# Optimization experiments

Hardware: AMD Instinct MI355X
Metric: run time of the kernel (lower is better)

## Reference

```python
import jax, jax.numpy as jnp
import numpy as np

N_NODES = 50000


def _sage_conv(x, src, dst, Wl, bl, Wr):
    # mean aggregation of neighbor (source) features at destination nodes
    msg = x[src]                                              # [E, d]
    agg = jax.ops.segment_sum(msg, dst, num_segments=N_NODES)  # [N, d]
    cnt = jax.ops.segment_sum(jnp.ones((src.shape[0],), x.dtype), dst,
                              num_segments=N_NODES)            # [N]
    agg = agg / jnp.clip(cnt, 1.0)[:, None]
    # lin_l(aggregated) + lin_r(self), bias only on lin_l (PyG default)
    return agg @ Wl + bl + x @ Wr


def setup_inputs() -> dict:
    key = jax.random.key(0)
    ks = jax.random.split(key, 8)
    d = 128
    E = 800000
    x = jax.random.normal(ks[0], (N_NODES, d), dtype=jnp.float32)
    edge_index = jax.random.randint(ks[1], (2, E), 0, N_NODES, dtype=jnp.int64)
    s1 = 1.0 / np.sqrt(d)
    s2 = 1.0 / np.sqrt(32)
    return {
        "x": x,
        "edge_index": edge_index,
        "W1l": jax.random.normal(ks[2], (d, 32), jnp.float32) * s1,
        "b1": jnp.zeros((32,), jnp.float32),
        "W1r": jax.random.normal(ks[3], (d, 32), jnp.float32) * s1,
        "W2l": jax.random.normal(ks[4], (32, 32), jnp.float32) * s2,
        "b2": jnp.zeros((32,), jnp.float32),
        "W2r": jax.random.normal(ks[5], (32, 32), jnp.float32) * s2,
    }


def reference(x, edge_index, W1l, b1, W1r, W2l, b2, W2r):
    src, dst = edge_index[0], edge_index[1]
    h = jax.nn.relu(_sage_conv(x, src, dst, W1l, b1, W1r))
    return _sage_conv(h, src, dst, W2l, b2, W2r)
```

## Files before the change

### kernel.cpp

```cpp
#include <hip/hip_runtime.h>


#define N_NODES 50000
#define NB 782
#define BKS 64
#define GB 256
#define CAPE 1280

__global__ __launch_bounds__(256) void kproj(
    const float* __restrict__ in, const float* __restrict__ Wl,
    const float* __restrict__ Wr, float* __restrict__ z, int N, int K) {
  __shared__ float xs[64 * 68];
  __shared__ float ws[64 * 64];
  const int t = threadIdx.x;
  const int n0 = blockIdx.x * 64;
  const int nvalid = (N - n0) < 64 ? (N - n0) : 64;

  const int tx = t & 15, ty = t >> 4;
  const int c0 = tx * 4;
  const int nl = ty * 4;

  float acc[4][4];
#pragma unroll
  for (int i = 0; i < 4; i++)
#pragma unroll
    for (int j = 0; j < 4; j++) acc[i][j] = 0.f;

  for (int kc = 0; kc < K; kc += 64) {
    const int KC = (K - kc) < 64 ? (K - kc) : 64;
    for (int i = t; i < KC * 32; i += 256) {
      int k = i >> 5, c = i & 31;
      ws[k * 64 + c] = Wl[(size_t)(kc + k) * 32 + c];
      ws[k * 64 + 32 + c] = Wr[(size_t)(kc + k) * 32 + c];
    }
    {
      const int kq = KC >> 2;
      const int sh = (KC == 64) ? 4 : 3;
      const int lim = nvalid * kq;
      for (int i = t; i < lim; i += 256) {
        int n = i >> sh, q = i & (kq - 1);
        float4 v = *(const float4*)(in + (size_t)(n0 + n) * K + kc + q * 4);
        *(float4*)(xs + n * 68 + q * 4) = v;
      }
    }
    __syncthreads();

    const float* x0 = xs + (nl + 0) * 68;
    const float* x1 = xs + (nl + 1) * 68;
    const float* x2 = xs + (nl + 2) * 68;
    const float* x3 = xs + (nl + 3) * 68;
    for (int k = 0; k < KC; k += 4) {
      float4 xa = *(const float4*)(x0 + k);
      float4 xb = *(const float4*)(x1 + k);
      float4 xc = *(const float4*)(x2 + k);
      float4 xd = *(const float4*)(x3 + k);
#pragma unroll
      for (int kk = 0; kk < 4; kk++) {
        float4 w = *(const float4*)(ws + (k + kk) * 64 + c0);
        float va = ((const float*)&xa)[kk];
        float vb = ((const float*)&xb)[kk];
        float vc = ((const float*)&xc)[kk];
        float vd = ((const float*)&xd)[kk];
        acc[0][0] += va * w.x; acc[0][1] += va * w.y;
        acc[0][2] += va * w.z; acc[0][3] += va * w.w;
        acc[1][0] += vb * w.x; acc[1][1] += vb * w.y;
        acc[1][2] += vb * w.z; acc[1][3] += vb * w.w;
        acc[2][0] += vc * w.x; acc[2][1] += vc * w.y;
        acc[2][2] += vc * w.z; acc[2][3] += vc * w.w;
        acc[3][0] += vd * w.x; acc[3][1] += vd * w.y;
        acc[3][2] += vd * w.z; acc[3][3] += vd * w.w;
      }
    }
    __syncthreads();
  }
#pragma unroll
  for (int i = 0; i < 4; i++) {
    int node = n0 + nl + i;
    if (node < N) {
      float4 v = make_float4(acc[i][0], acc[i][1], acc[i][2], acc[i][3]);
      *(float4*)(z + (size_t)node * 64 + c0) = v;
    }
  }
}

__global__ __launch_bounds__(256) void k_bcount(const int* __restrict__ dst,
                                                int* __restrict__ blkhist,
                                                int E, int chunk) {
  __shared__ int h[NB];
  const int t = threadIdx.x, b = blockIdx.x;
  for (int i = t; i < NB; i += 256) h[i] = 0;
  __syncthreads();
  const int e0 = b * chunk;
  int e1 = e0 + chunk;
  if (e1 > E) e1 = E;
  for (int e = e0 + t; e < e1; e += 256) atomicAdd(&h[dst[e] >> 6], 1);
  __syncthreads();
  for (int i = t; i < NB; i += 256) blkhist[b * NB + i] = h[i];
}

__global__ __launch_bounds__(256) void k_bscan_col(int* __restrict__ blkhist,
                                                   int* __restrict__ tot) {
  const int c = blockIdx.x * 256 + threadIdx.x;
  if (c >= NB) return;
  int run = 0;
  for (int b = 0; b < GB; b += 8) {
    int v[8];
#pragma unroll
    for (int i = 0; i < 8; i++) v[i] = blkhist[(size_t)(b + i) * NB + c];
#pragma unroll
    for (int i = 0; i < 8; i++) {
      blkhist[(size_t)(b + i) * NB + c] = run;
      run += v[i];
    }
  }
  tot[c] = run;
}

__global__ __launch_bounds__(256) void k_bscan_bb(const int* __restrict__ tot,
                                                  int* __restrict__ bb, int E) {
  __shared__ int t4[1024];
  __shared__ int sc[256];
  const int t = threadIdx.x;
  for (int c = t; c < 1024; c += 256) t4[c] = (c < NB) ? tot[c] : 0;
  __syncthreads();
  const int base = 4 * t;
  int v0 = t4[base], v1 = t4[base + 1], v2 = t4[base + 2], v3 = t4[base + 3];
  int s = v0 + v1 + v2 + v3;
  sc[t] = s;
  __syncthreads();
  for (int off = 1; off < 256; off <<= 1) {
    int tmp = (t >= off) ? sc[t - off] : 0;
    __syncthreads();
    sc[t] += tmp;
    __syncthreads();
  }
  const int excl = sc[t] - s;
  if (base < NB) bb[base] = excl;
  if (base + 1 < NB) bb[base + 1] = excl + v0;
  if (base + 2 < NB) bb[base + 2] = excl + v0 + v1;
  if (base + 3 < NB) bb[base + 3] = excl + v0 + v1 + v2;
  if (t == 0) bb[NB] = E;
}

__global__ __launch_bounds__(256) void k_bscatter(
    const int* __restrict__ src, const int* __restrict__ dst,
    const int* __restrict__ blkhist, const int* __restrict__ bb,
    int* __restrict__ ebuf, int E, int chunk) {
  __shared__ int cur[NB];
  const int t = threadIdx.x, b = blockIdx.x;
  for (int i = t; i < NB; i += 256) cur[i] = bb[i] + blkhist[(size_t)b * NB + i];
  __syncthreads();
  const int e0 = b * chunk;
  int e1 = e0 + chunk;
  if (e1 > E) e1 = E;
  for (int e = e0 + t; e < e1; e += 256) {
    int d = dst[e], s = src[e];
    int pos = atomicAdd(&cur[d >> 6], 1);
    ebuf[pos] = (s << 6) | (d & 63);
  }
}

__global__ __launch_bounds__(512) void k_fagg1(
    const float* __restrict__ zc, const int* __restrict__ ebuf,
    const int* __restrict__ bb, const float* __restrict__ b1,
    const float* __restrict__ W2l, const float* __restrict__ W2r,
    float* __restrict__ z2, int N) {
  __shared__ int lds_e[CAPE];
  __shared__ int lds_s[CAPE];
  __shared__ int deg[BKS];
  __shared__ int cur[BKS];
  __shared__ int off[BKS];
  __shared__ float w2p[32 * 64];
  __shared__ float bsh[32];
  const int t = threadIdx.x;
  const int k = blockIdx.x;
  const int r0 = bb[k], r1 = bb[k + 1];
  int ne = r1 - r0;
  if (ne > CAPE) ne = CAPE;

  for (int i = t; i < ne; i += 512) lds_e[i] = ebuf[r0 + i];
  if (t < BKS) deg[t] = 0;
  for (int i = t; i < 2048; i += 512) {
    int jj = i >> 6, c = i & 63;
    w2p[i] = (c < 32) ? W2l[jj * 32 + c] : W2r[jj * 32 + (c - 32)];
  }
  if (t < 32) bsh[t] = b1[t];
  __syncthreads();

  for (int i = t; i < ne; i += 512) atomicAdd(&deg[lds_e[i] & 63], 1);
  __syncthreads();

  if (t < 64) {
    int d = deg[t];
    int x = d;
#pragma unroll
    for (int o = 1; o < 64; o <<= 1) {
      int y = __shfl_up(x, o, 64);
      if (t >= o) x += y;
    }
    off[t] = x - d;
    cur[t] = x - d;
  }
  __syncthreads();

  for (int i = t; i < ne; i += 512) {
    int v = lds_e[i];
    int p = atomicAdd(&cur[v & 63], 1);
    lds_s[p] = v >> 6;
  }
  __syncthreads();

  const int g = t >> 5, j = t & 31;
  const int n0 = k << 6;
#pragma unroll
  for (int i = 0; i < 4; i++) {
    const int nl = g * 4 + i;
    const int node = n0 + nl;
    if (node >= N) break;
    const int a = off[nl];
    const int dg = deg[nl];
    const int b = a + dg;
    float a0 = 0.f, a1 = 0.f, a2 = 0.f, a3 = 0.f;
    int e = a;
    for (; e + 4 <= b; e += 4) {
      int s0 = lds_s[e], s1 = lds_s[e + 1], s2 = lds_s[e + 2], s3 = lds_s[e + 3];
      a0 += zc[(size_t)s0 * 64 + j];
      a1 += zc[(size_t)s1 * 64 + j];
      a2 += zc[(size_t)s2 * 64 + j];
      a3 += zc[(size_t)s3 * 64 + j];
    }
    for (; e < b; ++e) a0 += zc[(size_t)lds_s[e] * 64 + j];
    float sum = (a0 + a1) + (a2 + a3);
    float h = sum / (float)(dg > 1 ? dg : 1) + bsh[j] +
              zc[(size_t)node * 64 + 32 + j];
    h = fmaxf(h, 0.f);
    float p0 = 0.f, p1 = 0.f;
#pragma unroll
    for (int jj = 0; jj < 32; jj++) {
      float hj = __shfl(h, jj, 32);
      p0 += hj * w2p[jj * 64 + j];
      p1 += hj * w2p[jj * 64 + 32 + j];
    }
    z2[(size_t)node * 64 + j] = p0;
    z2[(size_t)node * 64 + 32 + j] = p1;
  }
}

__global__ __launch_bounds__(512) void k_fagg2(
    const float* __restrict__ z2, const int* __restrict__ ebuf,
    const int* __restrict__ bb, const float* __restrict__ b2,
    float* __restrict__ out, int N) {
  __shared__ int lds_e[CAPE];
  __shared__ int lds_s[CAPE];
  __shared__ int deg[BKS];
  __shared__ int cur[BKS];
  __shared__ int off[BKS];
  __shared__ float bsh[32];
  const int t = threadIdx.x;
  const int k = blockIdx.x;
  const int r0 = bb[k], r1 = bb[k + 1];
  int ne = r1 - r0;
  if (ne > CAPE) ne = CAPE;

  for (int i = t; i < ne; i += 512) lds_e[i] = ebuf[r0 + i];
  if (t < BKS) deg[t] = 0;
  if (t < 32) bsh[t] = b2[t];
  __syncthreads();

  for (int i = t; i < ne; i += 512) atomicAdd(&deg[lds_e[i] & 63], 1);
  __syncthreads();

  if (t < 64) {
    int d = deg[t];
    int x = d;
#pragma unroll
    for (int o = 1; o < 64; o <<= 1) {
      int y = __shfl_up(x, o, 64);
      if (t >= o) x += y;
    }
    off[t] = x - d;
    cur[t] = x - d;
  }
  __syncthreads();

  for (int i = t; i < ne; i += 512) {
    int v = lds_e[i];
    int p = atomicAdd(&cur[v & 63], 1);
    lds_s[p] = v >> 6;
  }
  __syncthreads();

  const int g = t >> 5, j = t & 31;
  const int n0 = k << 6;
#pragma unroll
  for (int i = 0; i < 4; i++) {
    const int nl = g * 4 + i;
    const int node = n0 + nl;
    if (node >= N) break;
    const int a = off[nl];
    const int dg = deg[nl];
    const int b = a + dg;
    float a0 = 0.f, a1 = 0.f, a2 = 0.f, a3 = 0.f;
    int e = a;
    for (; e + 4 <= b; e += 4) {
      int s0 = lds_s[e], s1 = lds_s[e + 1], s2 = lds_s[e + 2], s3 = lds_s[e + 3];
      a0 += z2[(size_t)s0 * 64 + j];
      a1 += z2[(size_t)s1 * 64 + j];
      a2 += z2[(size_t)s2 * 64 + j];
      a3 += z2[(size_t)s3 * 64 + j];
    }
    for (; e < b; ++e) a0 += z2[(size_t)lds_s[e] * 64 + j];
    float sum = (a0 + a1) + (a2 + a3);
    float v = sum / (float)(dg > 1 ? dg : 1) + bsh[j] +
              z2[(size_t)node * 64 + 32 + j];
    out[(size_t)node * 32 + j] = v;
  }
}

extern "C" void kernel_launch(void* const* d_in, const int* in_sizes, int n_in,
                              void* d_out, int out_size, void* d_ws,
                              size_t ws_size, hipStream_t stream) {
  const float* x = (const float*)d_in[0];
  const int* ei = (const int*)d_in[1];
  const float* W1l = (const float*)d_in[2];
  const float* b1 = (const float*)d_in[3];
  const float* W1r = (const float*)d_in[4];
  const float* W2l = (const float*)d_in[5];
  const float* b2 = (const float*)d_in[6];
  const float* W2r = (const float*)d_in[7];
  float* out = (float*)d_out;

  const int N = N_NODES;
  const int E = in_sizes[1] / 2;

  float* zc = (float*)d_ws;
  float* zc2 = zc + (size_t)N * 64;
  int* ebuf = (int*)(zc2 + (size_t)N * 64);
  int* bb = ebuf + E;
  int* tot = bb + NB + 1;
  int* blkhist = tot + NB;

  const int* srcp = ei;
  const int* dstp = ei + E;

  const int chunk = (E + GB - 1) / GB;
  const int nblk_proj = (N + 63) / 64;

  k_bcount<<<GB, 256, 0, stream>>>(dstp, blkhist, E, chunk);
  k_bscan_col<<<(NB + 255) / 256, 256, 0, stream>>>(blkhist, tot);
  k_bscan_bb<<<1, 256, 0, stream>>>(tot, bb, E);
  k_bscatter<<<GB, 256, 0, stream>>>(srcp, dstp, blkhist, bb, ebuf, E, chunk);
  kproj<<<nblk_proj, 256, 0, stream>>>(x, W1l, W1r, zc, N, 128);
  k_fagg1<<<NB, 512, 0, stream>>>(zc, ebuf, bb, b1, W2l, W2r, zc2, N);
  k_fagg2<<<NB, 512, 0, stream>>>(zc2, ebuf, bb, b2, out, N);
}
```

Measured before the change: 180.2 us.

## Fuse edge bucketing with projection into one kernel using fixed-capacity buckets

Replaces the four-kernel count/scan/scan/scatter bucketing pipeline with fixed-capacity per-bucket slots (CAPE each), filled through global atomic counters. The bucketing blocks and the first-layer projection blocks run in a single launch and share LDS through a union. This removes several launches and the global prefix-scan passes. In exchange it adds global atomics per tile and bucket, edge order inside a bucket becomes nondeterministic, and edges beyond CAPE per bucket are silently dropped. Packing src and dst into 16 bits each assumes node ids below 65536.

```diff
diff --git a/kernel.cpp b/kernel.cpp
--- a/kernel.cpp
+++ b/kernel.cpp
@@ -6,16 +6,57 @@
 #define BKS 64
 #define GB 256
 #define CAPE 1280
-
-__global__ __launch_bounds__(256) void kproj(
+#define TILE 3200
+
+__global__ __launch_bounds__(256) void k_front(
     const float* __restrict__ in, const float* __restrict__ Wl,
-    const float* __restrict__ Wr, float* __restrict__ z, int N, int K) {
-  __shared__ float xs[64 * 68];
-  __shared__ float ws[64 * 64];
+    const float* __restrict__ Wr, float* __restrict__ z, int N, int K,
+    const int* __restrict__ src, const int* __restrict__ dst,
+    int* __restrict__ gcnt, int* __restrict__ ebuf, int E) {
+  __shared__ union {
+    struct { float xs[64 * 68]; float ws[64 * 64]; } p;
+    struct { unsigned pe[TILE]; int hist[NB]; int cur[NB]; } b;
+  } sm;
   const int t = threadIdx.x;
-  const int n0 = blockIdx.x * 64;
+
+  if (blockIdx.x < GB) {
+    const int chunk = (E + GB - 1) / GB;
+    const int e0 = blockIdx.x * chunk;
+    int e1 = e0 + chunk;
+    if (e1 > E) e1 = E;
+    for (int ts = e0; ts < e1; ts += TILE) {
+      int te = ts + TILE;
+      if (te > e1) te = e1;
+      const int n = te - ts;
+      for (int i = t; i < NB; i += 256) sm.b.hist[i] = 0;
+      __syncthreads();
+      for (int i = t; i < n; i += 256) {
+        unsigned s = (unsigned)src[ts + i];
+        unsigned d = (unsigned)dst[ts + i];
+        sm.b.pe[i] = (s << 16) | d;
+        atomicAdd(&sm.b.hist[d >> 6], 1);
+      }
+      __syncthreads();
+      for (int c = t; c < NB; c += 256) {
+        int h = sm.b.hist[c];
+        sm.b.cur[c] = h ? atomicAdd(&gcnt[c], h) : 0;
+      }
+      __syncthreads();
+      for (int i = t; i < n; i += 256) {
+        unsigned pe = sm.b.pe[i];
+        int d = (int)(pe & 0xFFFFu);
+        int s = (int)(pe >> 16);
+        int c = d >> 6;
+        int p = atomicAdd(&sm.b.cur[c], 1);
+        if (p < CAPE) ebuf[(size_t)c * CAPE + p] = (s << 6) | (d & 63);
+      }
+      __syncthreads();
+    }
+    return;
+  }
+
+  const int n0 = (blockIdx.x - GB) * 64;
   const int nvalid = (N - n0) < 64 ? (N - n0) : 64;
-
   const int tx = t & 15, ty = t >> 4;
   const int c0 = tx * 4;
   const int nl = ty * 4;
@@ -30,8 +71,8 @@
     const int KC = (K - kc) < 64 ? (K - kc) : 64;
     for (int i = t; i < KC * 32; i += 256) {
       int k = i >> 5, c = i & 31;
-      ws[k * 64 + c] = Wl[(size_t)(kc + k) * 32 + c];
-      ws[k * 64 + 32 + c] = Wr[(size_t)(kc + k) * 32 + c];
+      sm.p.ws[k * 64 + c] = Wl[(size_t)(kc + k) * 32 + c];
+      sm.p.ws[k * 64 + 32 + c] = Wr[(size_t)(kc + k) * 32 + c];
     }
     {
       const int kq = KC >> 2;
@@ -40,15 +81,15 @@
       for (int i = t; i < lim; i += 256) {
         int n = i >> sh, q = i & (kq - 1);
         float4 v = *(const float4*)(in + (size_t)(n0 + n) * K + kc + q * 4);
-        *(float4*)(xs + n * 68 + q * 4) = v;
+        *(float4*)(sm.p.xs + n * 68 + q * 4) = v;
       }
     }
     __syncthreads();
 
-    const float* x0 = xs + (nl + 0) * 68;
-    const float* x1 = xs + (nl + 1) * 68;
-    const float* x2 = xs + (nl + 2) * 68;
-    const float* x3 = xs + (nl + 3) * 68;
+    const float* x0 = sm.p.xs + (nl + 0) * 68;
+    const float* x1 = sm.p.xs + (nl + 1) * 68;
+    const float* x2 = sm.p.xs + (nl + 2) * 68;
+    const float* x3 = sm.p.xs + (nl + 3) * 68;
     for (int k = 0; k < KC; k += 4) {
       float4 xa = *(const float4*)(x0 + k);
       float4 xb = *(const float4*)(x1 + k);
@@ -56,7 +97,7 @@
       float4 xd = *(const float4*)(x3 + k);
 #pragma unroll
       for (int kk = 0; kk < 4; kk++) {
-        float4 w = *(const float4*)(ws + (k + kk) * 64 + c0);
+        float4 w = *(const float4*)(sm.p.ws + (k + kk) * 64 + c0);
         float va = ((const float*)&xa)[kk];
         float vb = ((const float*)&xb)[kk];
         float vc = ((const float*)&xc)[kk];
@@ -83,86 +124,9 @@
   }
 }
 
-__global__ __launch_bounds__(256) void k_bcount(const int* __restrict__ dst,
-                                                int* __restrict__ blkhist,
-                                                int E, int chunk) {
-  __shared__ int h[NB];
-  const int t = threadIdx.x, b = blockIdx.x;
-  for (int i = t; i < NB; i += 256) h[i] = 0;
-  __syncthreads();
-  const int e0 = b * chunk;
-  int e1 = e0 + chunk;
-  if (e1 > E) e1 = E;
-  for (int e = e0 + t; e < e1; e += 256) atomicAdd(&h[dst[e] >> 6], 1);
-  __syncthreads();
-  for (int i = t; i < NB; i += 256) blkhist[b * NB + i] = h[i];
-}
-
-__global__ __launch_bounds__(256) void k_bscan_col(int* __restrict__ blkhist,
-                                                   int* __restrict__ tot) {
-  const int c = blockIdx.x * 256 + threadIdx.x;
-  if (c >= NB) return;
-  int run = 0;
-  for (int b = 0; b < GB; b += 8) {
-    int v[8];
-#pragma unroll
-    for (int i = 0; i < 8; i++) v[i] = blkhist[(size_t)(b + i) * NB + c];
-#pragma unroll
-    for (int i = 0; i < 8; i++) {
-      blkhist[(size_t)(b + i) * NB + c] = run;
-      run += v[i];
-    }
-  }
-  tot[c] = run;
-}
-
-__global__ __launch_bounds__(256) void k_bscan_bb(const int* __restrict__ tot,
-                                                  int* __restrict__ bb, int E) {
-  __shared__ int t4[1024];
-  __shared__ int sc[256];
-  const int t = threadIdx.x;
-  for (int c = t; c < 1024; c += 256) t4[c] = (c < NB) ? tot[c] : 0;
-  __syncthreads();
-  const int base = 4 * t;
-  int v0 = t4[base], v1 = t4[base + 1], v2 = t4[base + 2], v3 = t4[base + 3];
-  int s = v0 + v1 + v2 + v3;
-  sc[t] = s;
-  __syncthreads();
-  for (int off = 1; off < 256; off <<= 1) {
-    int tmp = (t >= off) ? sc[t - off] : 0;
-    __syncthreads();
-    sc[t] += tmp;
-    __syncthreads();
-  }
-  const int excl = sc[t] - s;
-  if (base < NB) bb[base] = excl;
-  if (base + 1 < NB) bb[base + 1] = excl + v0;
-  if (base + 2 < NB) bb[base + 2] = excl + v0 + v1;
-  if (base + 3 < NB) bb[base + 3] = excl + v0 + v1 + v2;
-  if (t == 0) bb[NB] = E;
-}
-
-__global__ __launch_bounds__(256) void k_bscatter(
-    const int* __restrict__ src, const int* __restrict__ dst,
-    const int* __restrict__ blkhist, const int* __restrict__ bb,
-    int* __restrict__ ebuf, int E, int chunk) {
-  __shared__ int cur[NB];
-  const int t = threadIdx.x, b = blockIdx.x;
-  for (int i = t; i < NB; i += 256) cur[i] = bb[i] + blkhist[(size_t)b * NB + i];
-  __syncthreads();
-  const int e0 = b * chunk;
-  int e1 = e0 + chunk;
-  if (e1 > E) e1 = E;
-  for (int e = e0 + t; e < e1; e += 256) {
-    int d = dst[e], s = src[e];
-    int pos = atomicAdd(&cur[d >> 6], 1);
-    ebuf[pos] = (s << 6) | (d & 63);
-  }
-}
-
 __global__ __launch_bounds__(512) void k_fagg1(
     const float* __restrict__ zc, const int* __restrict__ ebuf,
-    const int* __restrict__ bb, const float* __restrict__ b1,
+    const int* __restrict__ gcnt, const float* __restrict__ b1,
     const float* __restrict__ W2l, const float* __restrict__ W2r,
     float* __restrict__ z2, int N) {
   __shared__ int lds_e[CAPE];
@@ -174,11 +138,11 @@
   __shared__ float bsh[32];
   const int t = threadIdx.x;
   const int k = blockIdx.x;
-  const int r0 = bb[k], r1 = bb[k + 1];
-  int ne = r1 - r0;
+  int ne = gcnt[k];
   if (ne > CAPE) ne = CAPE;
-
-  for (int i = t; i < ne; i += 512) lds_e[i] = ebuf[r0 + i];
+  const size_t base = (size_t)k * CAPE;
+
+  for (int i = t; i < ne; i += 512) lds_e[i] = ebuf[base + i];
   if (t < BKS) deg[t] = 0;
   for (int i = t; i < 2048; i += 512) {
     int jj = i >> 6, c = i & 63;
@@ -248,7 +212,7 @@
 
 __global__ __launch_bounds__(512) void k_fagg2(
     const float* __restrict__ z2, const int* __restrict__ ebuf,
-    const int* __restrict__ bb, const float* __restrict__ b2,
+    const int* __restrict__ gcnt, const float* __restrict__ b2,
     float* __restrict__ out, int N) {
   __shared__ int lds_e[CAPE];
   __shared__ int lds_s[CAPE];
@@ -258,11 +222,11 @@
   __shared__ float bsh[32];
   const int t = threadIdx.x;
   const int k = blockIdx.x;
-  const int r0 = bb[k], r1 = bb[k + 1];
-  int ne = r1 - r0;
+  int ne = gcnt[k];
   if (ne > CAPE) ne = CAPE;
-
-  for (int i = t; i < ne; i += 512) lds_e[i] = ebuf[r0 + i];
+  const size_t base = (size_t)k * CAPE;
+
+  for (int i = t; i < ne; i += 512) lds_e[i] = ebuf[base + i];
   if (t < BKS) deg[t] = 0;
   if (t < 32) bsh[t] = b2[t];
   __syncthreads();
@@ -336,21 +300,16 @@
   float* zc = (float*)d_ws;
   float* zc2 = zc + (size_t)N * 64;
   int* ebuf = (int*)(zc2 + (size_t)N * 64);
-  int* bb = ebuf + E;
-  int* tot = bb + NB + 1;
-  int* blkhist = tot + NB;
+  int* gcnt = ebuf + (size_t)NB * CAPE;
 
   const int* srcp = ei;
   const int* dstp = ei + E;
 
-  const int chunk = (E + GB - 1) / GB;
   const int nblk_proj = (N + 63) / 64;
 
-  k_bcount<<<GB, 256, 0, stream>>>(dstp, blkhist, E, chunk);
-  k_bscan_col<<<(NB + 255) / 256, 256, 0, stream>>>(blkhist, tot);
-  k_bscan_bb<<<1, 256, 0, stream>>>(tot, bb, E);
-  k_bscatter<<<GB, 256, 0, stream>>>(srcp, dstp, blkhist, bb, ebuf, E, chunk);
-  kproj<<<nblk_proj, 256, 0, stream>>>(x, W1l, W1r, zc, N, 128);
-  k_fagg1<<<NB, 512, 0, stream>>>(zc, ebuf, bb, b1, W2l, W2r, zc2, N);
-  k_fagg2<<<NB, 512, 0, stream>>>(zc2, ebuf, bb, b2, out, N);
+  hipMemsetAsync(gcnt, 0, NB * sizeof(int), stream);
+  k_front<<<GB + nblk_proj, 256, 0, stream>>>(x, W1l, W1r, zc, N, 128, srcp,
+                                              dstp, gcnt, ebuf, E);
+  k_fagg1<<<NB, 512, 0, stream>>>(zc, ebuf, gcnt, b1, W2l, W2r, zc2, N);
+  k_fagg2<<<NB, 512, 0, stream>>>(zc2, ebuf, gcnt, b2, out, N);
 }
```

Measured after the change: 171.1 us. 1.05x faster.
